# Performance work log

Hardware: AMD Instinct MI355X
Metric: run time of the kernel (lower is better)

Reference implementation:

```python
import jax, jax.numpy as jnp
import numpy as np

B, S, E, H, V, T = 64, 64, 256, 512, 50000, 32
SOS, PAD = 1, 0


def setup_inputs() -> dict:
    key = jax.random.key(0)
    ks = jax.random.split(key, 12)
    sc = 0.05
    embedding = jax.random.normal(ks[0], (V, E), jnp.float32) * sc
    embedding = embedding.at[PAD].set(0.0)  # padding_idx row is zero
    inp = {
        "encoder_hidden": jax.random.normal(ks[1], (1, B, H), jnp.float32),
        "target": jax.random.randint(ks[2], (B, T), 0, V),
        "target_length": jax.random.randint(ks[3], (B,), 1, T + 1),
        "encoder_outputs": jax.random.normal(ks[4], (B, S, H), jnp.float32),
        "embedding": embedding,
        "w_ih": jax.random.normal(ks[5], (3 * H, E), jnp.float32) * sc,
        "w_hh": jax.random.normal(ks[6], (3 * H, H), jnp.float32) * sc,
        "b_ih": jnp.zeros((3 * H,), jnp.float32),
        "b_hh": jnp.zeros((3 * H,), jnp.float32),
        "attn_w": jax.random.normal(ks[7], (H, H), jnp.float32) * sc,  # Attention 'general' W
        "Wa": jax.random.normal(ks[8], (H, 2 * H), jnp.float32) * sc,  # concat projection (no bias)
        "fc_w": jax.random.normal(ks[9], (V, H), jnp.float32) * sc,
        "fc_b": jnp.zeros((V,), jnp.float32),
    }
    return inp


def _gru_cell(x, h, w_ih, w_hh, b_ih, b_hh):
    # PyTorch GRU cell math. x: [B,E], h: [B,H]
    gi = x @ w_ih.T + b_ih          # [B,3H]
    gh = h @ w_hh.T + b_hh          # [B,3H]
    i_r, i_z, i_n = jnp.split(gi, 3, axis=-1)
    h_r, h_z, h_n = jnp.split(gh, 3, axis=-1)
    r = jax.nn.sigmoid(i_r + h_r)
    z = jax.nn.sigmoid(i_z + h_z)
    n = jnp.tanh(i_n + r * h_n)
    return (1.0 - z) * n + z * h


def reference(encoder_hidden, target, target_length, encoder_outputs, embedding,
              w_ih, w_hh, b_ih, b_hh, attn_w, Wa, fc_w, fc_b):
    h0 = encoder_hidden[0]                                   # [B,H]
    # Luong 'general' attention: precompute W_attn @ encoder_outputs once
    enc_proj = jnp.einsum("bsh,gh->bsg", encoder_outputs, attn_w)  # [B,S,H]
    init_input = jnp.full((B,), SOS, dtype=jnp.int32)

    def step(carry, _):
        dec_in, h = carry
        x = embedding[dec_in]                                # [B,E]
        h_new = _gru_cell(x, h, w_ih, w_hh, b_ih, b_hh)      # [B,H]
        scores = jnp.einsum("bh,bsh->bs", h_new, enc_proj)   # [B,S]
        attn_weights = jax.nn.softmax(scores, axis=-1)
        context = jnp.einsum("bs,bsh->bh", attn_weights, encoder_outputs)
        concat = jnp.concatenate([h_new, context], axis=-1)  # [B,2H]
        concat_out = jnp.tanh(concat @ Wa.T)                 # [B,H]
        logits = jax.nn.log_softmax(concat_out @ fc_w.T + fc_b, axis=-1)  # [B,V]
        nxt = jnp.argmax(logits, axis=-1).astype(jnp.int32)  # topk(1) -> greedy
        return (nxt, h_new), logits

    (_, h_fin), outs = jax.lax.scan(step, (init_input, h0), None, length=T)
    decoder_outputs = jnp.transpose(outs, (1, 0, 2))          # [B,T,V]
    return decoder_outputs, h_fin[None]                       # ([B,T,V], [1,B,H])
```

## Files before the change

### kernel.cpp

```cpp
#include <hip/hip_runtime.h>
#include <hip/hip_bf16.h>
#include <math.h>

#define B_ 64
#define S_ 64
#define E_ 256
#define H_ 512
#define V_ 50000
#define T_ 32
#define SOS_ 1
#define NCHUNK 196
#define MARGIN 0.25f
static const long long LDCV = (long long)T_ * V_;

typedef unsigned short u16;
typedef unsigned long long u64;
typedef u16   u16x8  __attribute__((ext_vector_type(8)));
typedef short bf16x8 __attribute__((ext_vector_type(8)));
typedef float f32x4  __attribute__((ext_vector_type(4)));

static __device__ __forceinline__ u16 f2bf(float f) {
    unsigned u = __float_as_uint(f);
    unsigned r = (u + 0x7FFFu + ((u >> 16) & 1u)) >> 16;
    return (u16)r;
}
static __device__ __forceinline__ unsigned pk2(float a, float b) {
    __hip_bfloat162 t = __float22bfloat162_rn(make_float2(a, b));
    unsigned r; __builtin_memcpy(&r, &t, 4); return r;
}
static __device__ __forceinline__ unsigned fenc(float f) {
    unsigned u = __float_as_uint(f);
    return u ^ ((u & 0x80000000u) ? 0xFFFFFFFFu : 0x80000000u);
}
static __device__ __forceinline__ float fdec(unsigned e) {
    unsigned u = (e & 0x80000000u) ? (e ^ 0x80000000u) : ~e;
    return __uint_as_float(u);
}

__global__ __launch_bounds__(256) void build_wbig(
    const float* __restrict__ w_ih, const float* __restrict__ w_hh,
    const float* __restrict__ b_ih, const float* __restrict__ b_hh,
    float* __restrict__ WbigT, float* __restrict__ biasBig)
{
    int g = blockIdx.x * 256 + threadIdx.x;
    if (g < 2048 * 768) {
        int n = g / 768, k = g % 768;
        int j = n >> 2, c = n & 3;
        float v = 0.f;
        if (c == 0)      v = (k < 256) ? w_ih[j * 256 + k]          : w_hh[j * 512 + (k - 256)];
        else if (c == 1) v = (k < 256) ? w_ih[(512 + j) * 256 + k]  : w_hh[(512 + j) * 512 + (k - 256)];
        else if (c == 2) v = (k < 256) ? w_ih[(1024 + j) * 256 + k] : 0.f;
        else             v = (k < 256) ? 0.f                        : w_hh[(1024 + j) * 512 + (k - 256)];
        WbigT[g] = v;
    }
    if (g < 2048) {
        int j = g >> 2, c = g & 3;
        float bv;
        if (c == 0)      bv = b_ih[j] + b_hh[j];
        else if (c == 1) bv = b_ih[512 + j] + b_hh[512 + j];
        else if (c == 2) bv = b_ih[1024 + j];
        else             bv = b_hh[1024 + j];
        biasBig[g] = bv;
    }
}

__global__ __launch_bounds__(256) void transpose_aw(
    const float* __restrict__ attn_w, float* __restrict__ awT)
{
    int idx = blockIdx.x * 256 + threadIdx.x;
    int h = idx >> 9, g = idx & 511;
    awT[idx] = attn_w[g * 512 + h];
}

__global__ __launch_bounds__(256) void init_state(
    const float* __restrict__ enc_hidden, float* __restrict__ hbuf0,
    u64* __restrict__ win64, unsigned* __restrict__ rowmax)
{
    int idx = blockIdx.x * 256 + threadIdx.x;
    if (idx < B_ * H_) hbuf0[idx] = enc_hidden[idx];
    if (idx < B_) {
        win64[idx] = (u64)(~(unsigned)SOS_);
        rowmax[idx] = 0u;
    }
}

__global__ __launch_bounds__(256) void conv_fcw(
    const float* __restrict__ fc_w, u16* __restrict__ fcwb)
{
    size_t i = (size_t)(blockIdx.x * 256 + threadIdx.x) * 8;
    float4 a = *(const float4*)&fc_w[i];
    float4 b = *(const float4*)&fc_w[i + 4];
    u16x8 o;
    o[0] = f2bf(a.x); o[1] = f2bf(a.y); o[2] = f2bf(a.z); o[3] = f2bf(a.w);
    o[4] = f2bf(b.x); o[5] = f2bf(b.y); o[6] = f2bf(b.z); o[7] = f2bf(b.w);
    *(u16x8*)&fcwb[i] = o;
}

__global__ __launch_bounds__(256) void gruh(
    const float* __restrict__ WbigT, const float* __restrict__ biasBig,
    const float* __restrict__ emb, const u64* __restrict__ win64,
    const float* __restrict__ hcur, float* __restrict__ hnxt,
    float* __restrict__ concatA)
{
    __shared__ float As[64][68];
    __shared__ float Ws[64][36];
    const int tid = threadIdx.x;
    const int n0 = blockIdx.x * 32;
    const int tm = tid & 31;
    const int tn = tid >> 5;
    float acc[2][4] = {{0.f}};
    int tokm[4];
    #pragma unroll
    for (int r = 0; r < 4; ++r) {
        int m = (tid + r * 256) >> 4;
        tokm[r] = (int)(~(unsigned)(win64[m] & 0xFFFFFFFFull));
    }

    for (int k0 = 0; k0 < 768; k0 += 64) {
        #pragma unroll
        for (int r = 0; r < 4; ++r) {
            int idx = tid + r * 256;
            int m = idx >> 4;
            int kk = (idx & 15) << 2;
            int k = k0 + kk;
            float4 v = (k < 256)
                ? *(const float4*)&emb[(size_t)tokm[r] * 256 + k]
                : *(const float4*)&hcur[m * 512 + (k - 256)];
            As[kk + 0][m] = v.x; As[kk + 1][m] = v.y;
            As[kk + 2][m] = v.z; As[kk + 3][m] = v.w;
        }
        #pragma unroll
        for (int r = 0; r < 2; ++r) {
            int idx = tid + r * 256;
            int n = idx >> 4;
            int kk = (idx & 15) << 2;
            float4 v = *(const float4*)&WbigT[(size_t)(n0 + n) * 768 + k0 + kk];
            Ws[kk + 0][n] = v.x; Ws[kk + 1][n] = v.y;
            Ws[kk + 2][n] = v.z; Ws[kk + 3][n] = v.w;
        }
        __syncthreads();
        #pragma unroll
        for (int kk = 0; kk < 64; ++kk) {
            float2 a = *(const float2*)&As[kk][tm << 1];
            float4 w = *(const float4*)&Ws[kk][tn << 2];
            acc[0][0] += a.x * w.x; acc[0][1] += a.x * w.y;
            acc[0][2] += a.x * w.z; acc[0][3] += a.x * w.w;
            acc[1][0] += a.y * w.x; acc[1][1] += a.y * w.y;
            acc[1][2] += a.y * w.z; acc[1][3] += a.y * w.w;
        }
        __syncthreads();
    }

    int jg = (n0 >> 2) + tn;
    float b0 = biasBig[(jg << 2) + 0], b1 = biasBig[(jg << 2) + 1];
    float b2 = biasBig[(jg << 2) + 2], b3 = biasBig[(jg << 2) + 3];
    #pragma unroll
    for (int i = 0; i < 2; ++i) {
        int m = (tm << 1) + i;
        float g0 = acc[i][0] + b0, g1 = acc[i][1] + b1;
        float g2 = acc[i][2] + b2, g3 = acc[i][3] + b3;
        float r_ = 1.f / (1.f + expf(-g0));
        float z_ = 1.f / (1.f + expf(-g1));
        float nn = tanhf(g2 + r_ * g3);
        float hv = hcur[m * 512 + jg];
        float h2 = (1.f - z_) * nn + z_ * hv;
        hnxt[m * 512 + jg] = h2;
        concatA[m * 1024 + jg] = h2;
    }
}

__global__ __launch_bounds__(256) void attnq(
    const float* __restrict__ hnew, const float* __restrict__ awT,
    const float* __restrict__ enc, float* __restrict__ concatA)
{
    int b = blockIdx.x, tid = threadIdx.x;
    __shared__ float hs[512], q[512], aw[64];
    hs[tid] = hnew[b * 512 + tid];
    hs[tid + 256] = hnew[b * 512 + 256 + tid];
    __syncthreads();
    #pragma unroll
    for (int hh = 0; hh < 2; ++hh) {
        int h = tid + hh * 256;
        const float4* wr = (const float4*)(awT + (size_t)h * 512);
        float a = 0.f;
        #pragma unroll 8
        for (int k = 0; k < 128; ++k) {
            float4 w4 = wr[k];
            a += hs[4 * k] * w4.x + hs[4 * k + 1] * w4.y
               + hs[4 * k + 2] * w4.z + hs[4 * k + 3] * w4.w;
        }
        q[h] = a;
    }
    __syncthreads();
    int wv = tid >> 6, ln = tid & 63;
    for (int si = 0; si < 16; ++si) {
        int s = wv * 16 + si;
        const float* er = enc + ((size_t)(b * 64 + s)) * 512;
        float p = 0.f;
        #pragma unroll
        for (int i = 0; i < 8; ++i) p += q[ln + (i << 6)] * er[ln + (i << 6)];
        for (int off = 32; off; off >>= 1) p += __shfl_down(p, off);
        if (ln == 0) aw[s] = p;
    }
    __syncthreads();
    if (tid < 64) {
        float v = aw[tid], m = v;
        for (int off = 32; off; off >>= 1) m = fmaxf(m, __shfl_xor(m, off));
        float e = __expf(v - m);
        float ssum = e;
        for (int off = 32; off; off >>= 1) ssum += __shfl_xor(ssum, off);
        aw[tid] = e / ssum;
    }
    __syncthreads();
    #pragma unroll
    for (int hh = 0; hh < 2; ++hh) {
        int h = tid + hh * 256;
        float c = 0.f;
        const float* eb = enc + (size_t)b * 64 * 512 + h;
        #pragma unroll 8
        for (int s = 0; s < 64; ++s) c += aw[s] * eb[s * 512];
        concatA[b * 1024 + 512 + h] = c;
    }
}

__global__ __launch_bounds__(256) void ctxtanh(
    const float* __restrict__ concatA, const float* __restrict__ Wa,
    float* __restrict__ Abuf, u16* __restrict__ Abufb,
    u64* __restrict__ win64, unsigned* __restrict__ rowmax)
{
    __shared__ float As[64][68];
    __shared__ float Ws[64][20];
    const int tid = threadIdx.x;
    const int n0 = blockIdx.x * 16;
    const int tm = tid & 63;
    const int tn = tid >> 6;
    if (blockIdx.x == 0 && tid < 64) {
        win64[tid] = 0ull;
        rowmax[tid] = 0u;
    }
    float acc[4] = {0.f, 0.f, 0.f, 0.f};

    for (int k0 = 0; k0 < 1024; k0 += 64) {
        #pragma unroll
        for (int r = 0; r < 4; ++r) {
            int idx = tid + r * 256;
            int m = idx >> 4;
            int kk = (idx & 15) << 2;
            float4 v = *(const float4*)&concatA[(size_t)m * 1024 + k0 + kk];
            As[kk + 0][m] = v.x; As[kk + 1][m] = v.y;
            As[kk + 2][m] = v.z; As[kk + 3][m] = v.w;
        }
        {
            int n = tid >> 4;
            int kk = (tid & 15) << 2;
            float4 v = *(const float4*)&Wa[(size_t)(n0 + n) * 1024 + k0 + kk];
            Ws[kk + 0][n] = v.x; Ws[kk + 1][n] = v.y;
            Ws[kk + 2][n] = v.z; Ws[kk + 3][n] = v.w;
        }
        __syncthreads();
        #pragma unroll
        for (int kk = 0; kk < 64; ++kk) {
            float a = As[kk][tm];
            float4 w = *(const float4*)&Ws[kk][tn << 2];
            acc[0] += a * w.x; acc[1] += a * w.y;
            acc[2] += a * w.z; acc[3] += a * w.w;
        }
        __syncthreads();
    }
    #pragma unroll
    for (int j2 = 0; j2 < 4; ++j2) {
        int n = n0 + (tn << 2) + j2;
        float th = tanhf(acc[j2]);
        Abuf[tm * 512 + n] = th;
        Abufb[tm * 512 + n] = f2bf(th);
    }
}

template <int CACHED>
__global__ __launch_bounds__(256) void logits_mfma(
    const u16* __restrict__ Abufb, const float* __restrict__ fcw,
    const u16* __restrict__ fcwb, const float* __restrict__ fc_b,
    float* __restrict__ outp, float* __restrict__ pmax,
    float* __restrict__ psum, unsigned* __restrict__ rowmax)
{
    __shared__ u16 sA[64 * 512];
    const int tid = threadIdx.x;
    const int wv = tid >> 6, lane = tid & 63;
    const int nb = blockIdx.x * 256;
    const int col16 = lane & 15, grp = lane >> 4;

    #pragma unroll
    for (int i = 0; i < 16; ++i) {
        int c = tid + i * 256;
        int m = c >> 6;
        int cb = (c & 63) << 4;
        int sb = cb ^ ((m & 7) << 4);
        *(u16x8*)((char*)sA + m * 1024 + sb) =
            *(const u16x8*)(Abufb + m * 512 + (cb >> 1));
    }
    __syncthreads();

    int nfb[4]; bool val[4];
    #pragma unroll
    for (int fn = 0; fn < 4; ++fn) {
        nfb[fn] = nb + wv * 64 + fn * 16;
        val[fn] = nfb[fn] < V_;
    }

    f32x4 acc[4][4];
    #pragma unroll
    for (int a = 0; a < 4; ++a)
        #pragma unroll
        for (int b2 = 0; b2 < 4; ++b2) acc[a][b2] = (f32x4){0.f, 0.f, 0.f, 0.f};

    if (CACHED) {
        const u16* wpb[4];
        #pragma unroll
        for (int fn = 0; fn < 4; ++fn) {
            size_t rowi = val[fn] ? (size_t)(nfb[fn] + col16) : 0;
            wpb[fn] = fcwb + rowi * 512 + (grp << 3);
        }
        bf16x8 bcur[4];
        #pragma unroll
        for (int fn = 0; fn < 4; ++fn) bcur[fn] = *(const bf16x8*)(wpb[fn]);
        for (int kt = 0; kt < 16; ++kt) {
            bf16x8 bnxt[4];
            int ktn = (kt < 15) ? kt + 1 : 15;
            #pragma unroll
            for (int fn = 0; fn < 4; ++fn)
                bnxt[fn] = *(const bf16x8*)(wpb[fn] + ktn * 32);
            bf16x8 af[4];
            int kb = kt * 64 + (grp << 4);
            #pragma unroll
            for (int fm = 0; fm < 4; ++fm) {
                int mg = fm * 16 + col16;
                af[fm] = *(const bf16x8*)((const char*)sA + mg * 1024 + (kb ^ ((mg & 7) << 4)));
            }
            #pragma unroll
            for (int fm = 0; fm < 4; ++fm)
                #pragma unroll
                for (int fn = 0; fn < 4; ++fn)
                    acc[fm][fn] = __builtin_amdgcn_mfma_f32_16x16x32_bf16(
                        af[fm], bcur[fn], acc[fm][fn], 0, 0, 0);
            #pragma unroll
            for (int fn = 0; fn < 4; ++fn) bcur[fn] = bnxt[fn];
        }
    } else {
        const float* wp[4];
        #pragma unroll
        for (int fn = 0; fn < 4; ++fn) {
            size_t rowi = val[fn] ? (size_t)(nfb[fn] + col16) : 0;
            wp[fn] = fcw + rowi * 512 + (grp << 3);
        }
        float4 lo[4], hi[4];
        #pragma unroll
        for (int fn = 0; fn < 4; ++fn) {
            lo[fn] = *(const float4*)(wp[fn]);
            hi[fn] = *(const float4*)(wp[fn] + 4);
        }
        for (int kt = 0; kt < 16; ++kt) {
            float4 nl[4], nh[4];
            int ktn = (kt < 15) ? kt + 1 : 15;
            #pragma unroll
            for (int fn = 0; fn < 4; ++fn) {
                nl[fn] = *(const float4*)(wp[fn] + ktn * 32);
                nh[fn] = *(const float4*)(wp[fn] + ktn * 32 + 4);
            }
            bf16x8 bc[4];
            #pragma unroll
            for (int fn = 0; fn < 4; ++fn) {
                union { unsigned u[4]; bf16x8 v; } cv;
                cv.u[0] = pk2(lo[fn].x, lo[fn].y);
                cv.u[1] = pk2(lo[fn].z, lo[fn].w);
                cv.u[2] = pk2(hi[fn].x, hi[fn].y);
                cv.u[3] = pk2(hi[fn].z, hi[fn].w);
                bc[fn] = cv.v;
            }
            bf16x8 af[4];
            int kb = kt * 64 + (grp << 4);
            #pragma unroll
            for (int fm = 0; fm < 4; ++fm) {
                int mg = fm * 16 + col16;
                af[fm] = *(const bf16x8*)((const char*)sA + mg * 1024 + (kb ^ ((mg & 7) << 4)));
            }
            #pragma unroll
            for (int fm = 0; fm < 4; ++fm)
                #pragma unroll
                for (int fn = 0; fn < 4; ++fn)
                    acc[fm][fn] = __builtin_amdgcn_mfma_f32_16x16x32_bf16(
                        af[fm], bc[fn], acc[fm][fn], 0, 0, 0);
            #pragma unroll
            for (int fn = 0; fn < 4; ++fn) { lo[fn] = nl[fn]; hi[fn] = nh[fn]; }
        }
    }
    __syncthreads();

    float* wmaxp = (float*)sA;
    float* wsump = (float*)(sA + 512);

    float bias[4];
    #pragma unroll
    for (int fn = 0; fn < 4; ++fn) bias[fn] = val[fn] ? fc_b[nfb[fn] + col16] : 0.f;

    #pragma unroll
    for (int fm = 0; fm < 4; ++fm) {
        #pragma unroll
        for (int r = 0; r < 4; ++r) {
            int mrow = fm * 16 + grp * 4 + r;
            float best = -INFINITY;
            float vv[4];
            #pragma unroll
            for (int fn = 0; fn < 4; ++fn) {
                float v = -INFINITY;
                if (val[fn]) {
                    v = acc[fm][fn][r] + bias[fn];
                    outp[(size_t)mrow * LDCV + nfb[fn] + col16] = v;
                    best = fmaxf(best, v);
                }
                vv[fn] = v;
            }
            #pragma unroll
            for (int d = 1; d < 16; d <<= 1) best = fmaxf(best, __shfl_xor(best, d));
            float s = 0.f;
            #pragma unroll
            for (int fn = 0; fn < 4; ++fn)
                if (val[fn]) s += __expf(vv[fn] - best);
            #pragma unroll
            for (int d = 1; d < 16; d <<= 1) s += __shfl_xor(s, d);
            if (col16 == 0) {
                wmaxp[wv * 64 + mrow] = best;
                wsump[wv * 64 + mrow] = s;
            }
        }
    }
    __syncthreads();
    if (tid < 64) {
        float gm = -INFINITY;
        #pragma unroll
        for (int w = 0; w < 4; ++w) gm = fmaxf(gm, wmaxp[w * 64 + tid]);
        float gs = 0.f;
        #pragma unroll
        for (int w = 0; w < 4; ++w)
            gs += wsump[w * 64 + tid] * __expf(wmaxp[w * 64 + tid] - gm);
        pmax[tid * NCHUNK + blockIdx.x] = gm;
        psum[tid * NCHUNK + blockIdx.x] = gs;
        atomicMax(rowmax + tid, fenc(gm));
    }
}

__global__ __launch_bounds__(256) void candrefine(
    const float* __restrict__ pmax, const float* __restrict__ psum,
    const float* __restrict__ out, const float* __restrict__ Abuf,
    const float* __restrict__ fcw, const float* __restrict__ fc_b,
    const unsigned* __restrict__ rowmax, u64* __restrict__ win64,
    float* __restrict__ logZ_arr, int t)
{
    const int c = blockIdx.x, b = blockIdx.y, tid = threadIdx.x;
    __shared__ float sv[256];

    float Mb = fdec(rowmax[b]);

    if (c == 0) {
        float pm_ = (tid < NCHUNK) ? pmax[b * NCHUNK + tid] : -INFINITY;
        sv[tid] = (tid < NCHUNK) ? psum[b * NCHUNK + tid] * __expf(pm_ - Mb) : 0.f;
        __syncthreads();
        for (int st = 128; st; st >>= 1) {
            if (tid < st) sv[tid] += sv[tid + st];
            __syncthreads();
        }
        if (tid == 0) logZ_arr[b * T_ + t] = Mb + logf(sv[0]);
        __syncthreads();
    }

    if (pmax[b * NCHUNK + c] < Mb - MARGIN) return;

    __shared__ float A[512];
    __shared__ u64 sp[256];
    A[tid] = Abuf[b * 512 + tid];
    A[tid + 256] = Abuf[b * 512 + 256 + tid];
    __syncthreads();

    u64 pk = 0ull;
    int n = c * 256 + tid;
    if (n < V_) {
        float L = out[(size_t)b * LDCV + (size_t)t * V_ + n];
        if (L >= Mb - MARGIN) {
            const float* wr = fcw + (size_t)n * 512;
            float d = fc_b[n];
            #pragma unroll 8
            for (int k = 0; k < 512; k += 4) {
                float4 w4 = *(const float4*)&wr[k];
                d += A[k] * w4.x + A[k + 1] * w4.y + A[k + 2] * w4.z + A[k + 3] * w4.w;
            }
            pk = ((u64)fenc(d) << 32) | (u64)(~(unsigned)n);
        }
    }
    sp[tid] = pk;
    __syncthreads();
    for (int st = 128; st; st >>= 1) {
        if (tid < st) { u64 o = sp[tid + st]; if (o > sp[tid]) sp[tid] = o; }
        __syncthreads();
    }
    if (tid == 0 && sp[0] != 0ull) atomicMax(&win64[b], sp[0]);
}

__global__ __launch_bounds__(256) void norm_all(
    float* __restrict__ out, const float* __restrict__ logZ_arr)
{
    int row = blockIdx.y;
    int j = blockIdx.x * 256 + threadIdx.x;
    if (j < 12500) {
        float z = logZ_arr[row];
        float4* p = (float4*)(out + (size_t)row * V_) + j;
        float4 v = *p;
        v.x -= z; v.y -= z; v.z -= z; v.w -= z;
        *p = v;
    }
}

__global__ __launch_bounds__(256) void final_copy(
    const float* __restrict__ hfin, float* __restrict__ dst)
{
    int idx = blockIdx.x * 256 + threadIdx.x;
    if (idx < B_ * H_) dst[idx] = hfin[idx];
}

extern "C" void kernel_launch(void* const* d_in, const int* in_sizes, int n_in,
                              void* d_out, int out_size, void* d_ws, size_t ws_size,
                              hipStream_t stream)
{
    const float* enc_hidden = (const float*)d_in[0];
    const float* enc    = (const float*)d_in[3];
    const float* emb    = (const float*)d_in[4];
    const float* w_ih   = (const float*)d_in[5];
    const float* w_hh   = (const float*)d_in[6];
    const float* b_ih   = (const float*)d_in[7];
    const float* b_hh   = (const float*)d_in[8];
    const float* attn_w = (const float*)d_in[9];
    const float* Wa     = (const float*)d_in[10];
    const float* fc_w   = (const float*)d_in[11];
    const float* fc_b   = (const float*)d_in[12];
    float* out = (float*)d_out;
    float* ws  = (float*)d_ws;

    size_t off = 0;
    float* WbigT   = ws + off; off += 1572864;
    float* biasBig = ws + off; off += 2048;
    float* awT     = ws + off; off += 262144;
    float* hbuf0   = ws + off; off += 32768;
    float* hbuf1   = ws + off; off += 32768;
    float* concatA = ws + off; off += 65536;
    float* Abuf    = ws + off; off += 32768;
    u16*   Abufb   = (u16*)(ws + off); off += 16384;
    float* pmax    = ws + off; off += 64 * NCHUNK;
    float* psum    = ws + off; off += 64 * NCHUNK;
    float* logZ_a  = ws + off; off += 64 * T_;
    unsigned* rowmax = (unsigned*)(ws + off); off += 64;
    u64*   win64   = (u64*)(ws + off); off += 128;
    off = (off + 3) & ~(size_t)3;
    u16*   fcwb    = (u16*)(ws + off);
    const bool big = ws_size >= (off + 12800000) * 4;

    build_wbig<<<6144, 256, 0, stream>>>(w_ih, w_hh, b_ih, b_hh, WbigT, biasBig);
    transpose_aw<<<1024, 256, 0, stream>>>(attn_w, awT);
    init_state<<<128, 256, 0, stream>>>(enc_hidden, hbuf0, win64, rowmax);
    if (big) conv_fcw<<<12500, 256, 0, stream>>>(fc_w, fcwb);

    for (int t = 0; t < T_; ++t) {
        float* hcur = (t & 1) ? hbuf1 : hbuf0;
        float* hnxt = (t & 1) ? hbuf0 : hbuf1;

        gruh<<<64, 256, 0, stream>>>(WbigT, biasBig, emb, win64, hcur, hnxt, concatA);
        attnq<<<64, 256, 0, stream>>>(hnxt, awT, enc, concatA);
        ctxtanh<<<32, 256, 0, stream>>>(concatA, Wa, Abuf, Abufb, win64, rowmax);
        if (big)
            logits_mfma<1><<<NCHUNK, 256, 0, stream>>>(
                Abufb, fc_w, fcwb, fc_b, out + (size_t)t * V_, pmax, psum, rowmax);
        else
            logits_mfma<0><<<NCHUNK, 256, 0, stream>>>(
                Abufb, fc_w, fcwb, fc_b, out + (size_t)t * V_, pmax, psum, rowmax);
        candrefine<<<dim3(NCHUNK, B_), 256, 0, stream>>>(
            pmax, psum, out, Abuf, fc_w, fc_b, rowmax, win64, logZ_a, t);
    }

    norm_all<<<dim3(49, 2048), 256, 0, stream>>>(out, logZ_a);
    final_copy<<<128, 256, 0, stream>>>(hbuf0, out + (size_t)B_ * T_ * V_);
}
```

Baseline: 5.498 ms.

## Fuse attention with concat projection and argmax refinement into logits kernel

Merges the attention kernel with the tanh(Wa·concat) projection so each batch row is handled by one block, removing the concatA round-trip and a launch per step. The greedy-argmax candidate refinement moves into the logits MFMA kernel. Each block now keeps near-max candidates against its own chunk max and rescores them exactly in fp32, instead of launching a separate 196x64-block candrefine kernel that re-reads the logits. The per-step logZ reduction is deferred to one kernel after the loop, using per-timestep pmax/psum buffers. In exchange, the Wa projection becomes a per-block matvec with less reuse, and chunk-local thresholds can produce more candidates to rescore.

```diff
diff --git a/kernel.cpp b/kernel.cpp
--- a/kernel.cpp
+++ b/kernel.cpp
@@ -11,6 +11,7 @@
 #define SOS_ 1
 #define NCHUNK 196
 #define MARGIN 0.25f
+#define CCAP 3072
 static const long long LDCV = (long long)T_ * V_;
 
 typedef unsigned short u16;
@@ -32,9 +33,20 @@
     unsigned u = __float_as_uint(f);
     return u ^ ((u & 0x80000000u) ? 0xFFFFFFFFu : 0x80000000u);
 }
-static __device__ __forceinline__ float fdec(unsigned e) {
-    unsigned u = (e & 0x80000000u) ? (e ^ 0x80000000u) : ~e;
-    return __uint_as_float(u);
+
+static __device__ __forceinline__ u64 exact_pack(
+    const float* __restrict__ Abuf, const float* __restrict__ fcw,
+    const float* __restrict__ fc_b, int mrow, int n)
+{
+    const float* Ar = Abuf + (size_t)mrow * 512;
+    const float* wr = fcw + (size_t)n * 512;
+    float d = fc_b[n];
+    #pragma unroll 8
+    for (int k = 0; k < 512; k += 4) {
+        float4 w4 = *(const float4*)&wr[k];
+        d += Ar[k] * w4.x + Ar[k + 1] * w4.y + Ar[k + 2] * w4.z + Ar[k + 3] * w4.w;
+    }
+    return ((u64)fenc(d) << 32) | (u64)(~(unsigned)n);
 }
 
 __global__ __launch_bounds__(256) void build_wbig(
@@ -74,14 +86,11 @@
 
 __global__ __launch_bounds__(256) void init_state(
     const float* __restrict__ enc_hidden, float* __restrict__ hbuf0,
-    u64* __restrict__ win64, unsigned* __restrict__ rowmax)
+    u64* __restrict__ win64)
 {
     int idx = blockIdx.x * 256 + threadIdx.x;
     if (idx < B_ * H_) hbuf0[idx] = enc_hidden[idx];
-    if (idx < B_) {
-        win64[idx] = (u64)(~(unsigned)SOS_);
-        rowmax[idx] = 0u;
-    }
+    if (idx < B_) win64[idx] = (u64)(~(unsigned)SOS_);
 }
 
 __global__ __launch_bounds__(256) void conv_fcw(
@@ -99,8 +108,7 @@
 __global__ __launch_bounds__(256) void gruh(
     const float* __restrict__ WbigT, const float* __restrict__ biasBig,
     const float* __restrict__ emb, const u64* __restrict__ win64,
-    const float* __restrict__ hcur, float* __restrict__ hnxt,
-    float* __restrict__ concatA)
+    const float* __restrict__ hcur, float* __restrict__ hnxt)
 {
     __shared__ float As[64][68];
     __shared__ float Ws[64][36];
@@ -165,18 +173,21 @@
         float hv = hcur[m * 512 + jg];
         float h2 = (1.f - z_) * nn + z_ * hv;
         hnxt[m * 512 + jg] = h2;
-        concatA[m * 1024 + jg] = h2;
-    }
-}
-
-__global__ __launch_bounds__(256) void attnq(
+    }
+}
+
+__global__ __launch_bounds__(256) void attnqctx(
     const float* __restrict__ hnew, const float* __restrict__ awT,
-    const float* __restrict__ enc, float* __restrict__ concatA)
+    const float* __restrict__ enc, const float* __restrict__ Wa,
+    float* __restrict__ Abuf, u16* __restrict__ Abufb,
+    u64* __restrict__ win64)
 {
     int b = blockIdx.x, tid = threadIdx.x;
-    __shared__ float hs[512], q[512], aw[64];
-    hs[tid] = hnew[b * 512 + tid];
-    hs[tid + 256] = hnew[b * 512 + 256 + tid];
+    __shared__ float cc[1024];
+    __shared__ float q[512], aw[64];
+    if (tid == 0) win64[b] = 0ull;
+    cc[tid] = hnew[b * 512 + tid];
+    cc[tid + 256] = hnew[b * 512 + 256 + tid];
     __syncthreads();
     #pragma unroll
     for (int hh = 0; hh < 2; ++hh) {
@@ -186,8 +197,8 @@
         #pragma unroll 8
         for (int k = 0; k < 128; ++k) {
             float4 w4 = wr[k];
-            a += hs[4 * k] * w4.x + hs[4 * k + 1] * w4.y
-               + hs[4 * k + 2] * w4.z + hs[4 * k + 3] * w4.w;
+            a += cc[4 * k] * w4.x + cc[4 * k + 1] * w4.y
+               + cc[4 * k + 2] * w4.z + cc[4 * k + 3] * w4.w;
         }
         q[h] = a;
     }
@@ -219,60 +230,22 @@
         const float* eb = enc + (size_t)b * 64 * 512 + h;
         #pragma unroll 8
         for (int s = 0; s < 64; ++s) c += aw[s] * eb[s * 512];
-        concatA[b * 1024 + 512 + h] = c;
-    }
-}
-
-__global__ __launch_bounds__(256) void ctxtanh(
-    const float* __restrict__ concatA, const float* __restrict__ Wa,
-    float* __restrict__ Abuf, u16* __restrict__ Abufb,
-    u64* __restrict__ win64, unsigned* __restrict__ rowmax)
-{
-    __shared__ float As[64][68];
-    __shared__ float Ws[64][20];
-    const int tid = threadIdx.x;
-    const int n0 = blockIdx.x * 16;
-    const int tm = tid & 63;
-    const int tn = tid >> 6;
-    if (blockIdx.x == 0 && tid < 64) {
-        win64[tid] = 0ull;
-        rowmax[tid] = 0u;
-    }
-    float acc[4] = {0.f, 0.f, 0.f, 0.f};
-
-    for (int k0 = 0; k0 < 1024; k0 += 64) {
-        #pragma unroll
-        for (int r = 0; r < 4; ++r) {
-            int idx = tid + r * 256;
-            int m = idx >> 4;
-            int kk = (idx & 15) << 2;
-            float4 v = *(const float4*)&concatA[(size_t)m * 1024 + k0 + kk];
-            As[kk + 0][m] = v.x; As[kk + 1][m] = v.y;
-            As[kk + 2][m] = v.z; As[kk + 3][m] = v.w;
-        }
-        {
-            int n = tid >> 4;
-            int kk = (tid & 15) << 2;
-            float4 v = *(const float4*)&Wa[(size_t)(n0 + n) * 1024 + k0 + kk];
-            Ws[kk + 0][n] = v.x; Ws[kk + 1][n] = v.y;
-            Ws[kk + 2][n] = v.z; Ws[kk + 3][n] = v.w;
-        }
-        __syncthreads();
-        #pragma unroll
-        for (int kk = 0; kk < 64; ++kk) {
-            float a = As[kk][tm];
-            float4 w = *(const float4*)&Ws[kk][tn << 2];
-            acc[0] += a * w.x; acc[1] += a * w.y;
-            acc[2] += a * w.z; acc[3] += a * w.w;
-        }
-        __syncthreads();
-    }
-    #pragma unroll
-    for (int j2 = 0; j2 < 4; ++j2) {
-        int n = n0 + (tn << 2) + j2;
-        float th = tanhf(acc[j2]);
-        Abuf[tm * 512 + n] = th;
-        Abufb[tm * 512 + n] = f2bf(th);
+        cc[512 + h] = c;
+    }
+    __syncthreads();
+    #pragma unroll
+    for (int hh = 0; hh < 2; ++hh) {
+        int n = tid + hh * 256;
+        const float* wr = Wa + (size_t)n * 1024;
+        float a = 0.f;
+        #pragma unroll 8
+        for (int k = 0; k < 1024; k += 4) {
+            float4 w4 = *(const float4*)&wr[k];
+            a += cc[k] * w4.x + cc[k + 1] * w4.y + cc[k + 2] * w4.z + cc[k + 3] * w4.w;
+        }
+        float th = tanhf(a);
+        Abuf[b * 512 + n] = th;
+        Abufb[b * 512 + n] = f2bf(th);
     }
 }
 
@@ -280,10 +253,15 @@
 __global__ __launch_bounds__(256) void logits_mfma(
     const u16* __restrict__ Abufb, const float* __restrict__ fcw,
     const u16* __restrict__ fcwb, const float* __restrict__ fc_b,
-    float* __restrict__ outp, float* __restrict__ pmax,
-    float* __restrict__ psum, unsigned* __restrict__ rowmax)
+    const float* __restrict__ Abuf, float* __restrict__ outp,
+    float* __restrict__ pmax, float* __restrict__ psum,
+    u64* __restrict__ win64)
 {
     __shared__ u16 sA[64 * 512];
+    __shared__ int cands[CCAP];
+    __shared__ u64 wbest[64];
+    __shared__ float gmrow[64];
+    __shared__ int ccount;
     const int tid = threadIdx.x;
     const int wv = tid >> 6, lane = tid & 63;
     const int nb = blockIdx.x * 256;
@@ -397,6 +375,8 @@
 
     float* wmaxp = (float*)sA;
     float* wsump = (float*)(sA + 512);
+    if (tid == 0) ccount = 0;
+    if (tid < 64) wbest[tid] = 0ull;
 
     float bias[4];
     #pragma unroll
@@ -444,64 +424,57 @@
             gs += wsump[w * 64 + tid] * __expf(wmaxp[w * 64 + tid] - gm);
         pmax[tid * NCHUNK + blockIdx.x] = gm;
         psum[tid * NCHUNK + blockIdx.x] = gs;
-        atomicMax(rowmax + tid, fenc(gm));
-    }
-}
-
-__global__ __launch_bounds__(256) void candrefine(
-    const float* __restrict__ pmax, const float* __restrict__ psum,
-    const float* __restrict__ out, const float* __restrict__ Abuf,
-    const float* __restrict__ fcw, const float* __restrict__ fc_b,
-    const unsigned* __restrict__ rowmax, u64* __restrict__ win64,
-    float* __restrict__ logZ_arr, int t)
-{
-    const int c = blockIdx.x, b = blockIdx.y, tid = threadIdx.x;
+        gmrow[tid] = gm;
+    }
+    __syncthreads();
+
+    #pragma unroll
+    for (int fm = 0; fm < 4; ++fm) {
+        #pragma unroll
+        for (int r = 0; r < 4; ++r) {
+            int mrow = fm * 16 + grp * 4 + r;
+            float thr = gmrow[mrow] - MARGIN;
+            #pragma unroll
+            for (int fn = 0; fn < 4; ++fn) {
+                if (val[fn]) {
+                    float v = acc[fm][fn][r] + bias[fn];
+                    if (v >= thr) {
+                        int slot = atomicAdd(&ccount, 1);
+                        int n = nfb[fn] + col16;
+                        if (slot < CCAP) cands[slot] = (mrow << 16) | n;
+                        else atomicMax(&wbest[mrow], exact_pack(Abuf, fcw, fc_b, mrow, n));
+                    }
+                }
+            }
+        }
+    }
+    __syncthreads();
+    int nc = min(ccount, CCAP);
+    for (int i = tid; i < nc; i += 256) {
+        int e = cands[i];
+        int mrow = e >> 16, n = e & 0xFFFF;
+        atomicMax(&wbest[mrow], exact_pack(Abuf, fcw, fc_b, mrow, n));
+    }
+    __syncthreads();
+    if (tid < 64 && wbest[tid] != 0ull) atomicMax(&win64[tid], wbest[tid]);
+}
+
+__global__ __launch_bounds__(256) void logz_kernel(
+    const float* __restrict__ pmaxT, const float* __restrict__ psumT,
+    float* __restrict__ logZ_arr)
+{
+    int t = blockIdx.x, b = blockIdx.y, tid = threadIdx.x;
     __shared__ float sv[256];
-
-    float Mb = fdec(rowmax[b]);
-
-    if (c == 0) {
-        float pm_ = (tid < NCHUNK) ? pmax[b * NCHUNK + tid] : -INFINITY;
-        sv[tid] = (tid < NCHUNK) ? psum[b * NCHUNK + tid] * __expf(pm_ - Mb) : 0.f;
-        __syncthreads();
-        for (int st = 128; st; st >>= 1) {
-            if (tid < st) sv[tid] += sv[tid + st];
-            __syncthreads();
-        }
-        if (tid == 0) logZ_arr[b * T_ + t] = Mb + logf(sv[0]);
-        __syncthreads();
-    }
-
-    if (pmax[b * NCHUNK + c] < Mb - MARGIN) return;
-
-    __shared__ float A[512];
-    __shared__ u64 sp[256];
-    A[tid] = Abuf[b * 512 + tid];
-    A[tid + 256] = Abuf[b * 512 + 256 + tid];
-    __syncthreads();
-
-    u64 pk = 0ull;
-    int n = c * 256 + tid;
-    if (n < V_) {
-        float L = out[(size_t)b * LDCV + (size_t)t * V_ + n];
-        if (L >= Mb - MARGIN) {
-            const float* wr = fcw + (size_t)n * 512;
-            float d = fc_b[n];
-            #pragma unroll 8
-            for (int k = 0; k < 512; k += 4) {
-                float4 w4 = *(const float4*)&wr[k];
-                d += A[k] * w4.x + A[k + 1] * w4.y + A[k + 2] * w4.z + A[k + 3] * w4.w;
-            }
-            pk = ((u64)fenc(d) << 32) | (u64)(~(unsigned)n);
-        }
-    }
-    sp[tid] = pk;
-    __syncthreads();
-    for (int st = 128; st; st >>= 1) {
-        if (tid < st) { u64 o = sp[tid + st]; if (o > sp[tid]) sp[tid] = o; }
-        __syncthreads();
-    }
-    if (tid == 0 && sp[0] != 0ull) atomicMax(&win64[b], sp[0]);
+    const float* pm = pmaxT + ((size_t)t * 64 + b) * NCHUNK;
+    const float* ps = psumT + ((size_t)t * 64 + b) * NCHUNK;
+    float p = (tid < NCHUNK) ? pm[tid] : -INFINITY;
+    sv[tid] = p; __syncthreads();
+    for (int st = 128; st; st >>= 1) { if (tid < st) sv[tid] = fmaxf(sv[tid], sv[tid + st]); __syncthreads(); }
+    float Mb = sv[0]; __syncthreads();
+    sv[tid] = (tid < NCHUNK) ? ps[tid] * __expf(p - Mb) : 0.f;
+    __syncthreads();
+    for (int st = 128; st; st >>= 1) { if (tid < st) sv[tid] += sv[tid + st]; __syncthreads(); }
+    if (tid == 0) logZ_arr[b * T_ + t] = Mb + logf(sv[0]);
 }
 
 __global__ __launch_bounds__(256) void norm_all(
@@ -549,13 +522,12 @@
     float* awT     = ws + off; off += 262144;
     float* hbuf0   = ws + off; off += 32768;
     float* hbuf1   = ws + off; off += 32768;
-    float* concatA = ws + off; off += 65536;
     float* Abuf    = ws + off; off += 32768;
     u16*   Abufb   = (u16*)(ws + off); off += 16384;
-    float* pmax    = ws + off; off += 64 * NCHUNK;
-    float* psum    = ws + off; off += 64 * NCHUNK;
+    float* pmaxT   = ws + off; off += (size_t)T_ * 64 * NCHUNK;
+    float* psumT   = ws + off; off += (size_t)T_ * 64 * NCHUNK;
     float* logZ_a  = ws + off; off += 64 * T_;
-    unsigned* rowmax = (unsigned*)(ws + off); off += 64;
+    off = (off + 1) & ~(size_t)1;
     u64*   win64   = (u64*)(ws + off); off += 128;
     off = (off + 3) & ~(size_t)3;
     u16*   fcwb    = (u16*)(ws + off);
@@ -563,26 +535,26 @@
 
     build_wbig<<<6144, 256, 0, stream>>>(w_ih, w_hh, b_ih, b_hh, WbigT, biasBig);
     transpose_aw<<<1024, 256, 0, stream>>>(attn_w, awT);
-    init_state<<<128, 256, 0, stream>>>(enc_hidden, hbuf0, win64, rowmax);
+    init_state<<<128, 256, 0, stream>>>(enc_hidden, hbuf0, win64);
     if (big) conv_fcw<<<12500, 256, 0, stream>>>(fc_w, fcwb);
 
     for (int t = 0; t < T_; ++t) {
         float* hcur = (t & 1) ? hbuf1 : hbuf0;
         float* hnxt = (t & 1) ? hbuf0 : hbuf1;
-
-        gruh<<<64, 256, 0, stream>>>(WbigT, biasBig, emb, win64, hcur, hnxt, concatA);
-        attnq<<<64, 256, 0, stream>>>(hnxt, awT, enc, concatA);
-        ctxtanh<<<32, 256, 0, stream>>>(concatA, Wa, Abuf, Abufb, win64, rowmax);
+        float* pmS = pmaxT + (size_t)t * 64 * NCHUNK;
+        float* psS = psumT + (size_t)t * 64 * NCHUNK;
+
+        gruh<<<64, 256, 0, stream>>>(WbigT, biasBig, emb, win64, hcur, hnxt);
+        attnqctx<<<64, 256, 0, stream>>>(hnxt, awT, enc, Wa, Abuf, Abufb, win64);
         if (big)
             logits_mfma<1><<<NCHUNK, 256, 0, stream>>>(
-                Abufb, fc_w, fcwb, fc_b, out + (size_t)t * V_, pmax, psum, rowmax);
+                Abufb, fc_w, fcwb, fc_b, Abuf, out + (size_t)t * V_, pmS, psS, win64);
         else
             logits_mfma<0><<<NCHUNK, 256, 0, stream>>>(
-                Abufb, fc_w, fcwb, fc_b, out + (size_t)t * V_, pmax, psum, rowmax);
-        candrefine<<<dim3(NCHUNK, B_), 256, 0, stream>>>(
-            pmax, psum, out, Abuf, fc_w, fc_b, rowmax, win64, logZ_a, t);
-    }
-
+                Abufb, fc_w, fcwb, fc_b, Abuf, out + (size_t)t * V_, pmS, psS, win64);
+    }
+
+    logz_kernel<<<dim3(T_, B_), 256, 0, stream>>>(pmaxT, psumT, logZ_a);
     norm_all<<<dim3(49, 2048), 256, 0, stream>>>(out, logZ_a);
     final_copy<<<128, 256, 0, stream>>>(hbuf0, out + (size_t)B_ * T_ * V_);
 }
```

After: 8.070 ms. 46.8% more time.
